# Optimization experiments

Measured on AMD Instinct MI355X. Metric: run time of the kernel, lower is better.

## Reference

```python
import jax, jax.numpy as jnp
import numpy as np

NOT_EPSILON = 1.0
W_SCALE = 0.05  # scaled randn init for numerical stability of swishmax logits

H, T, A, C = 8, 1024, 64, 256  # heads, key/query size, attention size, compress size


def swishmax(x, axis):
    m = jnp.max(x, axis=axis, keepdims=True)
    xe = x * jnp.exp(x - m)
    return xe / (jnp.sum(jnp.abs(xe), axis=axis, keepdims=True) + NOT_EPSILON)


def setup_inputs() -> dict:
    key = jax.random.key(0)
    ks = jax.random.split(key, 7)
    B, Q, K = 2, 2048, 2048
    return {
        "query_tokens": jax.random.normal(ks[0], (B, Q, T), dtype=jnp.float32),
        "key_tokens": jax.random.normal(ks[1], (B, K, T), dtype=jnp.float32),
        "key_down": jax.random.normal(ks[2], (H, T, A), dtype=jnp.float32) * W_SCALE,
        "query_down": jax.random.normal(ks[3], (H, T, A), dtype=jnp.float32) * W_SCALE,
        "query_down_bias": jax.random.normal(ks[4], (H, 1, A), dtype=jnp.float32) * W_SCALE,
        "value_down": jax.random.normal(ks[5], (H, T, C), dtype=jnp.float32) * W_SCALE,
        "value_up": jax.random.normal(ks[6], (H, C, T), dtype=jnp.float32) * W_SCALE,
    }


def reference(query_tokens, key_tokens, key_down, query_down, query_down_bias, value_down, value_up):
    # key/query projections: [B,K,T] x [H,T,A] -> [B,H,K,A]
    k = jnp.einsum('bkt,hta->bhka', key_tokens, key_down)
    q = jnp.einsum('bqt,hta->bhqa', query_tokens, query_down) + query_down_bias[None]  # [B,H,Q,A]
    # attention logits: key @ query^T -> [B,H,K,Q]
    logits = jnp.einsum('bhka,bhqa->bhkq', k, q)
    attn = swishmax(logits, axis=-2)  # normalized over keys (dim=-2)
    # sum_k key_tokens[b,k,:] * attn[b,h,k,q]  ==  [B,H,Q,T] (matmul form of the outer-product sum)
    vs = jnp.einsum('bhkq,bkt->bhqt', attn, key_tokens)
    # compress path: value_down then value_up
    vs = jnp.einsum('bhqc,hct->bhqt', jnp.einsum('bhqt,htc->bhqc', vs, value_down), value_up)
    return vs.sum(axis=1)  # sum over heads -> [B,Q,T]
```

## Files before the change

### kernel.cpp

```cpp
#include <hip/hip_runtime.h>
#include <hip/hip_fp16.h>
#include <math.h>


typedef _Float16 f16;
typedef _Float16 f16x4 __attribute__((ext_vector_type(4)));
typedef _Float16 f16x8 __attribute__((ext_vector_type(8)));
typedef short s16x4 __attribute__((ext_vector_type(4)));
typedef short bf16x8 __attribute__((ext_vector_type(8)));
typedef float f32x4 __attribute__((ext_vector_type(4)));

#define MFMA_F16(a, b, c) __builtin_amdgcn_mfma_f32_16x16x32_f16(a, b, c, 0, 0, 0)
#define MFMA_BF16(a, b, c) __builtin_amdgcn_mfma_f32_16x16x32_bf16(a, b, c, 0, 0, 0)

__device__ __forceinline__ void g2lds16(const void* g, void* l) {
  __builtin_amdgcn_global_load_lds((__attribute__((address_space(1))) void*)g,
                                   (__attribute__((address_space(3))) void*)l, 16, 0, 0);
}

__device__ __forceinline__ short f32_bf16(float x) {
  union { float f; unsigned u; } v; v.f = x;
  unsigned r = v.u + 0x7FFFu + ((v.u >> 16) & 1u);
  return (short)(r >> 16);
}
__device__ __forceinline__ float bf16_f32(short h) {
  union { unsigned u; float f; } v; v.u = ((unsigned)(unsigned short)h) << 16;
  return v.f;
}

__global__ __launch_bounds__(256) void ew_split(const float* __restrict__ in,
                                                short* __restrict__ bhi,
                                                short* __restrict__ blo,
                                                f16* __restrict__ fo, int n4) {
  int i = blockIdx.x * 256 + threadIdx.x;
  int stride = gridDim.x * 256;
  for (; i < n4; i += stride) {
    f32x4 v = ((const f32x4*)in)[i];
    s16x4 h, l;
    f16x4 f;
#pragma unroll
    for (int j = 0; j < 4; j++) {
      short hj = f32_bf16(v[j]);
      h[j] = hj;
      l[j] = f32_bf16(v[j] - bf16_f32(hj));
      f[j] = (f16)v[j];
    }
    ((s16x4*)bhi)[i] = h;
    ((s16x4*)blo)[i] = l;
    if (fo) ((f16x4*)fo)[i] = f;
  }
}

__global__ __launch_bounds__(256) void transpose_split(const float* __restrict__ in,
                                                       short* __restrict__ bhi,
                                                       short* __restrict__ blo,
                                                       f16* __restrict__ fo,
                                                       int R, int C) {
  __shared__ float t[64][65];
  int cb = blockIdx.x * 64, rb = blockIdx.y * 64;
  size_t batch = (size_t)blockIdx.z * R * C;
  int tid = threadIdx.x;
#pragma unroll
  for (int i = 0; i < 4; i++) {
    int r = (tid >> 4) + i * 16, c4 = (tid & 15) * 4;
    f32x4 v = *(const f32x4*)(in + batch + (size_t)(rb + r) * C + cb + c4);
    t[r][c4] = v[0]; t[r][c4 + 1] = v[1]; t[r][c4 + 2] = v[2]; t[r][c4 + 3] = v[3];
  }
  __syncthreads();
#pragma unroll
  for (int i = 0; i < 4; i++) {
    int c = (tid >> 4) + i * 16, r4 = (tid & 15) * 4;
    float v0 = t[r4][c], v1 = t[r4 + 1][c], v2 = t[r4 + 2][c], v3 = t[r4 + 3][c];
    size_t o = batch + (size_t)(cb + c) * R + rb + r4;
    if (bhi) {
      s16x4 h = {f32_bf16(v0), f32_bf16(v1), f32_bf16(v2), f32_bf16(v3)};
      *(s16x4*)(bhi + o) = h;
      s16x4 l = {f32_bf16(v0 - bf16_f32(h[0])), f32_bf16(v1 - bf16_f32(h[1])),
                 f32_bf16(v2 - bf16_f32(h[2])), f32_bf16(v3 - bf16_f32(h[3]))};
      *(s16x4*)(blo + o) = l;
    }
    if (fo) {
      f16x4 fv = {(f16)v0, (f16)v1, (f16)v2, (f16)v3};
      *(f16x4*)(fo + o) = fv;
    }
  }
}

__global__ __launch_bounds__(256, 2) void proj_gemm(
    const short* __restrict__ qtok_hi, const short* __restrict__ qtok_lo,
    const short* __restrict__ ktok_hi, const short* __restrict__ ktok_lo,
    const short* __restrict__ wqT_hi, const short* __restrict__ wqT_lo,
    const short* __restrict__ wkT_hi, const short* __restrict__ wkT_lo,
    const float* __restrict__ bias, short* __restrict__ q_split,
    short* __restrict__ k_split) {
  const bool isQ = (blockIdx.z == 0);
  const short* Ahi = isQ ? qtok_hi : ktok_hi;
  const short* Alo = isQ ? qtok_lo : ktok_lo;
  const short* Bhi = isQ ? wqT_hi : wkT_hi;
  const short* Blo = isQ ? wqT_lo : wkT_lo;
  short* outp = isQ ? q_split : k_split;

  __shared__ __attribute__((aligned(16))) short sm[2][12288];

  int tid = threadIdx.x, w = tid >> 6, lane = tid & 63, g = lane >> 4, li = lane & 15;
  int mb = blockIdx.y * 64, nb = blockIdx.x * 128;
  int wm = (w >> 1) * 32, wn = (w & 1) * 64;

  f32x4 acc[2][4] = {};

  auto STAGE = [&](int kb, int buf) {
    {
      int off = tid * 16;
      int row = off >> 6, ss = ((off >> 4) & 3) ^ ((row >> 1) & 3);
      size_t src = (size_t)(mb + row) * 1024 + kb + ss * 8;
      g2lds16(Ahi + src, (char*)&sm[buf][0] + w * 1024);
      g2lds16(Alo + src, (char*)&sm[buf][2048] + w * 1024);
    }
#pragma unroll
    for (int i = 0; i < 2; i++) {
      int off = i * 4096 + tid * 16;
      int row = off >> 6, ss = ((off >> 4) & 3) ^ ((row >> 1) & 3);
      size_t src = (size_t)(nb + row) * 1024 + kb + ss * 8;
      g2lds16(Bhi + src, (char*)&sm[buf][4096] + i * 4096 + w * 1024);
      g2lds16(Blo + src, (char*)&sm[buf][8192] + i * 4096 + w * 1024);
    }
  };

  STAGE(0, 0);
  __syncthreads();
  for (int kb = 0; kb < 1024; kb += 32) {
    int cur = (kb >> 5) & 1;
    if (kb + 32 < 1024) STAGE(kb + 32, cur ^ 1);
    bf16x8 af[2][2], bf[4][2];
#pragma unroll
    for (int f = 0; f < 2; f++) {
      int ra = wm + f * 16 + li, sa = g ^ ((ra >> 1) & 3);
      af[f][0] = *(const bf16x8*)&sm[cur][ra * 32 + sa * 8];
      af[f][1] = *(const bf16x8*)&sm[cur][2048 + ra * 32 + sa * 8];
    }
#pragma unroll
    for (int f = 0; f < 4; f++) {
      int rb = wn + f * 16 + li, sb = g ^ ((rb >> 1) & 3);
      bf[f][0] = *(const bf16x8*)&sm[cur][4096 + rb * 32 + sb * 8];
      bf[f][1] = *(const bf16x8*)&sm[cur][8192 + rb * 32 + sb * 8];
    }
#pragma unroll
    for (int mf = 0; mf < 2; mf++)
#pragma unroll
      for (int nf = 0; nf < 4; nf++) {
        acc[mf][nf] = MFMA_BF16(af[mf][0], bf[nf][0], acc[mf][nf]);
        acc[mf][nf] = MFMA_BF16(af[mf][0], bf[nf][1], acc[mf][nf]);
        acc[mf][nf] = MFMA_BF16(af[mf][1], bf[nf][0], acc[mf][nf]);
      }
    __syncthreads();
  }
#pragma unroll
  for (int mf = 0; mf < 2; mf++)
#pragma unroll
    for (int nf = 0; nf < 4; nf++)
#pragma unroll
      for (int r = 0; r < 4; r++) {
        int m = mb + wm + mf * 16 + 4 * g + r;
        int n = nb + wn + nf * 16 + li;
        float v = acc[mf][nf][r];
        if (isQ) v += bias[n];
        short hi = f32_bf16(v);
        short lo = f32_bf16(v - bf16_f32(hi));
        size_t base = ((size_t)((m >> 11) * 8 + (n >> 6)) * 2048 + (m & 2047)) * 128;
        outp[base + (n & 63)] = hi;
        outp[base + 64 + (n & 63)] = lo;
      }
}

__global__ __launch_bounds__(256, 4) void kv_gemm(const f16* __restrict__ A,
                                                  const f16* __restrict__ Bm,
                                                  f16* __restrict__ kvT) {
  __shared__ __attribute__((aligned(16))) f16 sm[2][6144];
  int tid = threadIdx.x, w = tid >> 6, lane = tid & 63, g = lane >> 4, li = lane & 15;
  int mb = blockIdx.y * 64, nb = blockIdx.x * 128;
  int wm = (w >> 1) * 32, wn = (w & 1) * 64;
  f32x4 acc[2][4] = {};

  auto STAGE = [&](int kb, int buf) {
    {
      int off = tid * 16;
      int row = off >> 6, ss = ((off >> 4) & 3) ^ ((row >> 1) & 3);
      g2lds16(A + (size_t)(mb + row) * 1024 + kb + ss * 8, (char*)&sm[buf][0] + w * 1024);
    }
#pragma unroll
    for (int i = 0; i < 2; i++) {
      int off = i * 4096 + tid * 16;
      int row = off >> 6, ss = ((off >> 4) & 3) ^ ((row >> 1) & 3);
      g2lds16(Bm + (size_t)(nb + row) * 1024 + kb + ss * 8,
              (char*)&sm[buf][2048] + i * 4096 + w * 1024);
    }
  };

  STAGE(0, 0);
  __syncthreads();
  for (int kb = 0; kb < 1024; kb += 32) {
    int cur = (kb >> 5) & 1;
    if (kb + 32 < 1024) STAGE(kb + 32, cur ^ 1);
    f16x8 af[2], bf[4];
#pragma unroll
    for (int f = 0; f < 2; f++) {
      int ra = wm + f * 16 + li, sa = g ^ ((ra >> 1) & 3);
      af[f] = *(const f16x8*)&sm[cur][ra * 32 + sa * 8];
    }
#pragma unroll
    for (int f = 0; f < 4; f++) {
      int rb = wn + f * 16 + li, sb = g ^ ((rb >> 1) & 3);
      bf[f] = *(const f16x8*)&sm[cur][2048 + rb * 32 + sb * 8];
    }
#pragma unroll
    for (int mf = 0; mf < 2; mf++)
#pragma unroll
      for (int nf = 0; nf < 4; nf++)
        acc[mf][nf] = MFMA_F16(af[mf], bf[nf], acc[mf][nf]);
    __syncthreads();
  }
#pragma unroll
  for (int mf = 0; mf < 2; mf++)
#pragma unroll
    for (int nf = 0; nf < 4; nf++) {
      int m = mb + wm + mf * 16 + 4 * g;
      int n = nb + wn + nf * 16 + li;
      f16x4 v = {(f16)acc[mf][nf][0], (f16)acc[mf][nf][1], (f16)acc[mf][nf][2],
                 (f16)acc[mf][nf][3]};
      int bh = (m >> 11) * 8 + (n >> 8);
      size_t o = (size_t)bh * 524288 + (size_t)((m & 2047) >> 5) * 8192 +
                 (size_t)(n & 255) * 32 + (m & 31);
      *(f16x4*)(kvT + o) = v;
    }
}

__global__ __launch_bounds__(256, 2) void flash_attn(const short* __restrict__ q_split,
                                                     const short* __restrict__ k_split,
                                                     const f16* __restrict__ kvT,
                                                     f16* __restrict__ vs_c) {
  __shared__ __attribute__((aligned(16))) short k_lds[2][4096];
  __shared__ __attribute__((aligned(16))) f16 kv_lds[2][8192];
  __shared__ __attribute__((aligned(16))) f16 p_lds[2][4096];
  __shared__ float sc_lds[2][4][16];
  __shared__ float fix_lds[64];

  const int bid = blockIdx.x;
  const int bh = ((bid & 7) << 1) + ((bid >> 3) & 1);
  const int qb = bid >> 4;
  const int tid = threadIdx.x;
  const int w = tid >> 6, lane = tid & 63, g = lane >> 4, li = lane & 15;

  const short* qrow = q_split + ((size_t)bh * 2048 + qb * 64 + w * 16 + li) * 128;
  bf16x8 qf[2][2];
#pragma unroll
  for (int ach = 0; ach < 2; ach++)
#pragma unroll
    for (int hl = 0; hl < 2; hl++)
      qf[ach][hl] = *(const bf16x8*)(qrow + hl * 64 + ach * 32 + g * 8);

  const short* kbase = k_split + (size_t)bh * 262144;
  const f16* kvbase = kvT + (size_t)bh * 524288;

  float m_cur = -INFINITY, m_true = -INFINITY, l_run = 0.f;
  f32x4 acc[4][4] = {};

  auto STAGE_K = [&](int kt, int buf) {
#pragma unroll
    for (int i = 0; i < 2; i++) {
      int off = (w * 2 + i) * 1024 + lane * 16;
      int row = off >> 8;
      int ss = ((off >> 4) & 15) ^ (row & 7);
      g2lds16(kbase + kt * 4096 + row * 128 + ss * 8,
              (char*)k_lds[buf] + (w * 2 + i) * 1024);
    }
  };
  auto STAGE_KV = [&](int kt, int buf) {
#pragma unroll
    for (int i = 0; i < 4; i++) {
      int off = (w * 4 + i) * 1024 + lane * 16;
      int c = off >> 6;
      int ss = ((off >> 4) & 3) ^ ((c >> 1) & 3);
      g2lds16(kvbase + kt * 8192 + c * 32 + ss * 8,
              (char*)kv_lds[buf] + (w * 4 + i) * 1024);
    }
  };

  auto QKSM = [&](int buf) {
    f32x4 s[2] = {};
    __builtin_amdgcn_s_setprio(1);
#pragma unroll
    for (int kc = 0; kc < 2; kc++) {
      const int r = kc * 16 + li;
#pragma unroll
      for (int ach = 0; ach < 2; ach++) {
        int sh = (ach * 4 + g) ^ (r & 7);
        int sl = (8 + ach * 4 + g) ^ (r & 7);
        bf16x8 khi = *(const bf16x8*)((const char*)k_lds[buf] + r * 256 + sh * 16);
        bf16x8 klo = *(const bf16x8*)((const char*)k_lds[buf] + r * 256 + sl * 16);
        s[kc] = MFMA_BF16(khi, qf[ach][0], s[kc]);
        s[kc] = MFMA_BF16(khi, qf[ach][1], s[kc]);
        s[kc] = MFMA_BF16(klo, qf[ach][0], s[kc]);
      }
    }
    __builtin_amdgcn_s_setprio(0);

    float tmax = fmaxf(fmaxf(fmaxf(s[0][0], s[0][1]), fmaxf(s[0][2], s[0][3])),
                       fmaxf(fmaxf(s[1][0], s[1][1]), fmaxf(s[1][2], s[1][3])));
    tmax = fmaxf(tmax, __shfl_xor(tmax, 16));
    tmax = fmaxf(tmax, __shfl_xor(tmax, 32));
    m_true = fmaxf(m_true, tmax);
    float sc = 1.0f;
    if (__any(tmax > m_cur + 4.0f)) {
      float mn = fmaxf(m_cur, tmax);
      sc = __expf(m_cur - mn);
      l_run *= sc;
      m_cur = mn;
    }
    if (g == 0) sc_lds[buf][w][li] = sc;

    float ls = 0.f;
    float pv[8];
#pragma unroll
    for (int kc = 0; kc < 2; kc++)
#pragma unroll
      for (int r2 = 0; r2 < 4; r2++) {
        float sv = s[kc][r2];
        float e = sv * __expf(sv - m_cur);
        pv[kc * 4 + r2] = e;
        ls += fabsf(e);
      }
    ls += __shfl_xor(ls, 16);
    ls += __shfl_xor(ls, 32);
    l_run += ls;

#pragma unroll
    for (int kc = 0; kc < 2; kc++) {
      f16x4 p4 = {(f16)pv[kc * 4], (f16)pv[kc * 4 + 1], (f16)pv[kc * 4 + 2],
                  (f16)pv[kc * 4 + 3]};
      int wb = ((w * 16 + li) * 128 + kc * 32 + g * 8) ^ ((li & 7) << 4);
      *(f16x4*)((char*)p_lds[buf] + wb) = p4;
    }
  };

  STAGE_K(0, 0);
  STAGE_KV(0, 0);
  STAGE_K(1, 1);
  __syncthreads();
  QKSM(0);

#pragma unroll 2
  for (int kt = 0; kt < 64; kt++) {
    const int cur = kt & 1;
    __syncthreads();
    if (kt < 63) STAGE_KV(kt + 1, cur ^ 1);
    if (kt < 62) STAGE_K(kt + 2, cur);

    f16x8 kvf[4];
#pragma unroll
    for (int ct = 0; ct < 4; ct++) {
      int c = w * 64 + ct * 16 + li;
      int ss = g ^ ((c >> 1) & 3);
      kvf[ct] = *(const f16x8*)((const char*)kv_lds[cur] + c * 64 + ss * 16);
    }

    if (kt < 63) QKSM(cur ^ 1);

#pragma unroll
    for (int qt = 0; qt < 4; qt++) {
      float scq = sc_lds[cur][qt][li];
      if (__any(scq != 1.0f)) {
#pragma unroll
        for (int ct = 0; ct < 4; ct++) acc[ct][qt] *= scq;
      }
    }

    __builtin_amdgcn_s_setprio(1);
#pragma unroll
    for (int qt = 0; qt < 4; qt++) {
      int rb = ((qt * 16 + li) * 128 + g * 16) ^ ((li & 7) << 4);
      f16x8 pf = *(const f16x8*)((const char*)p_lds[cur] + rb);
#pragma unroll
      for (int ct = 0; ct < 4; ct++) acc[ct][qt] = MFMA_F16(kvf[ct], pf, acc[ct][qt]);
    }
    __builtin_amdgcn_s_setprio(0);
  }

  float sfix = __expf(m_cur - m_true);
  float invd = sfix / (l_run * sfix + 1.0f);
  __syncthreads();
  if (g == 0) fix_lds[w * 16 + li] = invd;
  __syncthreads();
#pragma unroll
  for (int qt = 0; qt < 4; qt++) {
    float iv = fix_lds[qt * 16 + li];
    f16* orow = vs_c + ((size_t)(bh >> 3) * 2048 + qb * 64 + qt * 16 + li) * 2048 +
                (bh & 7) * 256 + w * 64 + g * 4;
#pragma unroll
    for (int ct = 0; ct < 4; ct++) {
      f16x4 v = {(f16)(acc[ct][qt][0] * iv), (f16)(acc[ct][qt][1] * iv),
                 (f16)(acc[ct][qt][2] * iv), (f16)(acc[ct][qt][3] * iv)};
      *(f16x4*)(orow + ct * 16) = v;
    }
  }
}

__global__ __launch_bounds__(256, 2) void final_gemm(const f16* __restrict__ A,
                                                     const f16* __restrict__ Bm,
                                                     float* __restrict__ outp) {
  __shared__ __attribute__((aligned(16))) f16 sm[2][6144];
  int tid = threadIdx.x, w = tid >> 6, lane = tid & 63, g = lane >> 4, li = lane & 15;
  int mb = blockIdx.y * 64, nb = blockIdx.x * 128;
  int wm = (w >> 1) * 32, wn = (w & 1) * 64;
  f32x4 acc[2][4] = {};

  auto STAGE = [&](int kb, int buf) {
    {
      int off = tid * 16;
      int row = off >> 6, ss = ((off >> 4) & 3) ^ ((row >> 1) & 3);
      g2lds16(A + (size_t)(mb + row) * 2048 + kb + ss * 8, (char*)&sm[buf][0] + w * 1024);
    }
#pragma unroll
    for (int i = 0; i < 2; i++) {
      int off = i * 4096 + tid * 16;
      int row = off >> 6, ss = ((off >> 4) & 3) ^ ((row >> 1) & 3);
      g2lds16(Bm + (size_t)(nb + row) * 2048 + kb + ss * 8,
              (char*)&sm[buf][2048] + i * 4096 + w * 1024);
    }
  };

  STAGE(0, 0);
  __syncthreads();
  for (int kb = 0; kb < 2048; kb += 32) {
    int cur = (kb >> 5) & 1;
    if (kb + 32 < 2048) STAGE(kb + 32, cur ^ 1);
    f16x8 af[2], bf[4];
#pragma unroll
    for (int f = 0; f < 2; f++) {
      int ra = wm + f * 16 + li, sa = g ^ ((ra >> 1) & 3);
      af[f] = *(const f16x8*)&sm[cur][ra * 32 + sa * 8];
    }
#pragma unroll
    for (int f = 0; f < 4; f++) {
      int rb = wn + f * 16 + li, sb = g ^ ((rb >> 1) & 3);
      bf[f] = *(const f16x8*)&sm[cur][2048 + rb * 32 + sb * 8];
    }
#pragma unroll
    for (int mf = 0; mf < 2; mf++)
#pragma unroll
      for (int nf = 0; nf < 4; nf++)
        acc[mf][nf] = MFMA_F16(af[mf], bf[nf], acc[mf][nf]);
    __syncthreads();
  }
#pragma unroll
  for (int mf = 0; mf < 2; mf++)
#pragma unroll
    for (int nf = 0; nf < 4; nf++)
#pragma unroll
      for (int r = 0; r < 4; r++) {
        int m = mb + wm + mf * 16 + 4 * g + r;
        int n = nb + wn + nf * 16 + li;
        outp[(size_t)m * 1024 + n] = acc[mf][nf][r];
      }
}

extern "C" void kernel_launch(void* const* d_in, const int* in_sizes, int n_in,
                              void* d_out, int out_size, void* d_ws, size_t ws_size,
                              hipStream_t stream) {
  (void)in_sizes; (void)n_in; (void)out_size; (void)ws_size;
  const float* qtok = (const float*)d_in[0];
  const float* ktok = (const float*)d_in[1];
  const float* kdw = (const float*)d_in[2];
  const float* qdw = (const float*)d_in[3];
  const float* qdb = (const float*)d_in[4];
  const float* vdw = (const float*)d_in[5];
  const float* vup = (const float*)d_in[6];

  char* ws = (char*)d_ws;
  size_t off = 0;
  auto take = [&](size_t n) { void* p = ws + off; off += (n + 255) & ~(size_t)255; return p; };

  short* qtok_hi = (short*)take(8u << 20);
  short* qtok_lo = (short*)take(8u << 20);
  short* ktok_hi = (short*)take(8u << 20);
  short* ktok_lo = (short*)take(8u << 20);
  f16* ktok_f = (f16*)take(8u << 20);
  short* wqT_hi = (short*)take(1u << 20);
  short* wqT_lo = (short*)take(1u << 20);
  short* wkT_hi = (short*)take(1u << 20);
  short* wkT_lo = (short*)take(1u << 20);
  f16* vdT = (f16*)take(4u << 20);
  f16* vuT = (f16*)take(4u << 20);
  short* q_split = (short*)take(8u << 20);
  short* k_split = (short*)take(8u << 20);
  f16* kvT = (f16*)(void*)ktok_hi;
  f16* vs_c = (f16*)(void*)qtok_hi;

  ew_split<<<2048, 256, 0, stream>>>(qtok, qtok_hi, qtok_lo, (f16*)nullptr, 1048576);
  ew_split<<<2048, 256, 0, stream>>>(ktok, ktok_hi, ktok_lo, ktok_f, 1048576);
  transpose_split<<<dim3(1, 16, 8), 256, 0, stream>>>(qdw, wqT_hi, wqT_lo, nullptr, 1024, 64);
  transpose_split<<<dim3(1, 16, 8), 256, 0, stream>>>(kdw, wkT_hi, wkT_lo, nullptr, 1024, 64);
  transpose_split<<<dim3(4, 16, 8), 256, 0, stream>>>(vdw, nullptr, nullptr, vdT, 1024, 256);
  transpose_split<<<dim3(16, 32, 1), 256, 0, stream>>>(vup, nullptr, nullptr, vuT, 2048, 1024);

  proj_gemm<<<dim3(4, 64, 2), 256, 0, stream>>>(qtok_hi, qtok_lo, ktok_hi, ktok_lo,
                                                wqT_hi, wqT_lo, wkT_hi, wkT_lo, qdb,
                                                q_split, k_split);
  kv_gemm<<<dim3(16, 64), 256, 0, stream>>>(ktok_f, vdT, kvT);
  flash_attn<<<512, 256, 0, stream>>>(q_split, k_split, kvT, vs_c);
  final_gemm<<<dim3(8, 64), 256, 0, stream>>>(vs_c, vuT, (float*)d_out);
}
```

Measured before the change: 228.0 us.

## Load KV fragments directly to registers, double key tile, fuse preprocessing launches

```diff
diff --git a/kernel.cpp b/kernel.cpp
--- a/kernel.cpp
+++ b/kernel.cpp
@@ -28,37 +28,69 @@
   return v.f;
 }
 
-__global__ __launch_bounds__(256) void ew_split(const float* __restrict__ in,
-                                                short* __restrict__ bhi,
-                                                short* __restrict__ blo,
-                                                f16* __restrict__ fo, int n4) {
+__global__ __launch_bounds__(256) void ew_split2(const float* __restrict__ qin,
+                                                 const float* __restrict__ kin,
+                                                 short* __restrict__ qhi,
+                                                 short* __restrict__ qlo,
+                                                 short* __restrict__ khi,
+                                                 short* __restrict__ klo,
+                                                 f16* __restrict__ kf) {
   int i = blockIdx.x * 256 + threadIdx.x;
-  int stride = gridDim.x * 256;
-  for (; i < n4; i += stride) {
-    f32x4 v = ((const f32x4*)in)[i];
-    s16x4 h, l;
-    f16x4 f;
-#pragma unroll
-    for (int j = 0; j < 4; j++) {
-      short hj = f32_bf16(v[j]);
-      h[j] = hj;
-      l[j] = f32_bf16(v[j] - bf16_f32(hj));
-      f[j] = (f16)v[j];
-    }
-    ((s16x4*)bhi)[i] = h;
-    ((s16x4*)blo)[i] = l;
-    if (fo) ((f16x4*)fo)[i] = f;
-  }
-}
-
-__global__ __launch_bounds__(256) void transpose_split(const float* __restrict__ in,
-                                                       short* __restrict__ bhi,
-                                                       short* __restrict__ blo,
-                                                       f16* __restrict__ fo,
-                                                       int R, int C) {
+  const bool isK = i >= 1048576;
+  const int j = isK ? i - 1048576 : i;
+  const float* in = isK ? kin : qin;
+  f32x4 v = ((const f32x4*)in)[j];
+  s16x4 h, l;
+  f16x4 f;
+#pragma unroll
+  for (int e = 0; e < 4; e++) {
+    short he = f32_bf16(v[e]);
+    h[e] = he;
+    l[e] = f32_bf16(v[e] - bf16_f32(he));
+    f[e] = (f16)v[e];
+  }
+  if (isK) {
+    ((s16x4*)khi)[j] = h;
+    ((s16x4*)klo)[j] = l;
+    ((f16x4*)kf)[j] = f;
+  } else {
+    ((s16x4*)qhi)[j] = h;
+    ((s16x4*)qlo)[j] = l;
+  }
+}
+
+__global__ __launch_bounds__(256) void transpose_all(
+    const float* __restrict__ qdw, const float* __restrict__ kdw,
+    const float* __restrict__ vdw, const float* __restrict__ vup,
+    short* __restrict__ wqT_hi, short* __restrict__ wqT_lo,
+    short* __restrict__ wkT_hi, short* __restrict__ wkT_lo,
+    f16* __restrict__ vdT, f16* __restrict__ vuT) {
   __shared__ float t[64][65];
-  int cb = blockIdx.x * 64, rb = blockIdx.y * 64;
-  size_t batch = (size_t)blockIdx.z * R * C;
+  int idx = blockIdx.x;
+  const float* in;
+  short *bhi = nullptr, *blo = nullptr;
+  f16* fo = nullptr;
+  int R, C, cb, rb;
+  size_t batch;
+  if (idx < 256) {
+    bool isQ = idx < 128;
+    int i = isQ ? idx : idx - 128;
+    in = isQ ? qdw : kdw;
+    bhi = isQ ? wqT_hi : wkT_hi;
+    blo = isQ ? wqT_lo : wkT_lo;
+    R = 1024; C = 64; cb = 0; rb = (i & 15) * 64;
+    batch = (size_t)(i >> 4) * R * C;
+  } else if (idx < 768) {
+    int i = idx - 256;
+    in = vdw; fo = vdT;
+    R = 1024; C = 256; cb = (i & 3) * 64; rb = ((i >> 2) & 15) * 64;
+    batch = (size_t)(i >> 6) * R * C;
+  } else {
+    int i = idx - 768;
+    in = vup; fo = vuT;
+    R = 2048; C = 1024; cb = (i & 15) * 64; rb = (i >> 4) * 64;
+    batch = 0;
+  }
   int tid = threadIdx.x;
 #pragma unroll
   for (int i = 0; i < 4; i++) {
@@ -238,8 +270,7 @@
                                                      const short* __restrict__ k_split,
                                                      const f16* __restrict__ kvT,
                                                      f16* __restrict__ vs_c) {
-  __shared__ __attribute__((aligned(16))) short k_lds[2][4096];
-  __shared__ __attribute__((aligned(16))) f16 kv_lds[2][8192];
+  __shared__ __attribute__((aligned(16))) short k_lds[2][8192];
   __shared__ __attribute__((aligned(16))) f16 p_lds[2][4096];
   __shared__ float sc_lds[2][4][16];
   __shared__ float fix_lds[64];
@@ -259,37 +290,37 @@
       qf[ach][hl] = *(const bf16x8*)(qrow + hl * 64 + ach * 32 + g * 8);
 
   const short* kbase = k_split + (size_t)bh * 262144;
-  const f16* kvbase = kvT + (size_t)bh * 524288;
+  const f16* kvbase = kvT + (size_t)bh * 524288 + (size_t)w * 64 * 32 + li * 32 + g * 8;
 
   float m_cur = -INFINITY, m_true = -INFINITY, l_run = 0.f;
   f32x4 acc[4][4] = {};
-
-  auto STAGE_K = [&](int kt, int buf) {
-#pragma unroll
-    for (int i = 0; i < 2; i++) {
-      int off = (w * 2 + i) * 1024 + lane * 16;
+  f16x8 kvf[2][4];
+
+  auto STAGE_K = [&](int t, int buf) {
+#pragma unroll
+    for (int i = 0; i < 4; i++) {
+      int off = (w * 4 + i) * 1024 + lane * 16;
       int row = off >> 8;
       int ss = ((off >> 4) & 15) ^ (row & 7);
-      g2lds16(kbase + kt * 4096 + row * 128 + ss * 8,
-              (char*)k_lds[buf] + (w * 2 + i) * 1024);
+      g2lds16(kbase + t * 8192 + row * 128 + ss * 8,
+              (char*)k_lds[buf] + (w * 4 + i) * 1024);
     }
   };
-  auto STAGE_KV = [&](int kt, int buf) {
-#pragma unroll
-    for (int i = 0; i < 4; i++) {
-      int off = (w * 4 + i) * 1024 + lane * 16;
-      int c = off >> 6;
-      int ss = ((off >> 4) & 3) ^ ((c >> 1) & 3);
-      g2lds16(kvbase + kt * 8192 + c * 32 + ss * 8,
-              (char*)kv_lds[buf] + (w * 4 + i) * 1024);
+
+  auto LOADKV = [&](int t) {
+#pragma unroll
+    for (int h = 0; h < 2; h++) {
+      const f16* p = kvbase + (size_t)(2 * t + h) * 8192;
+#pragma unroll
+      for (int ct = 0; ct < 4; ct++) kvf[h][ct] = *(const f16x8*)(p + ct * 512);
     }
   };
 
   auto QKSM = [&](int buf) {
-    f32x4 s[2] = {};
+    f32x4 s[4] = {};
     __builtin_amdgcn_s_setprio(1);
 #pragma unroll
-    for (int kc = 0; kc < 2; kc++) {
+    for (int kc = 0; kc < 4; kc++) {
       const int r = kc * 16 + li;
 #pragma unroll
       for (int ach = 0; ach < 2; ach++) {
@@ -304,8 +335,10 @@
     }
     __builtin_amdgcn_s_setprio(0);
 
-    float tmax = fmaxf(fmaxf(fmaxf(s[0][0], s[0][1]), fmaxf(s[0][2], s[0][3])),
-                       fmaxf(fmaxf(s[1][0], s[1][1]), fmaxf(s[1][2], s[1][3])));
+    float tmax = -INFINITY;
+#pragma unroll
+    for (int kc = 0; kc < 4; kc++)
+      tmax = fmaxf(tmax, fmaxf(fmaxf(s[kc][0], s[kc][1]), fmaxf(s[kc][2], s[kc][3])));
     tmax = fmaxf(tmax, __shfl_xor(tmax, 16));
     tmax = fmaxf(tmax, __shfl_xor(tmax, 32));
     m_true = fmaxf(m_true, tmax);
@@ -319,9 +352,9 @@
     if (g == 0) sc_lds[buf][w][li] = sc;
 
     float ls = 0.f;
-    float pv[8];
-#pragma unroll
-    for (int kc = 0; kc < 2; kc++)
+    float pv[16];
+#pragma unroll
+    for (int kc = 0; kc < 4; kc++)
 #pragma unroll
       for (int r2 = 0; r2 < 4; r2++) {
         float sv = s[kc][r2];
@@ -334,7 +367,7 @@
     l_run += ls;
 
 #pragma unroll
-    for (int kc = 0; kc < 2; kc++) {
+    for (int kc = 0; kc < 4; kc++) {
       f16x4 p4 = {(f16)pv[kc * 4], (f16)pv[kc * 4 + 1], (f16)pv[kc * 4 + 2],
                   (f16)pv[kc * 4 + 3]};
       int wb = ((w * 16 + li) * 128 + kc * 32 + g * 8) ^ ((li & 7) << 4);
@@ -343,27 +376,17 @@
   };
 
   STAGE_K(0, 0);
-  STAGE_KV(0, 0);
   STAGE_K(1, 1);
   __syncthreads();
   QKSM(0);
 
 #pragma unroll 2
-  for (int kt = 0; kt < 64; kt++) {
-    const int cur = kt & 1;
+  for (int t = 0; t < 32; t++) {
+    const int cur = t & 1;
     __syncthreads();
-    if (kt < 63) STAGE_KV(kt + 1, cur ^ 1);
-    if (kt < 62) STAGE_K(kt + 2, cur);
-
-    f16x8 kvf[4];
-#pragma unroll
-    for (int ct = 0; ct < 4; ct++) {
-      int c = w * 64 + ct * 16 + li;
-      int ss = g ^ ((c >> 1) & 3);
-      kvf[ct] = *(const f16x8*)((const char*)kv_lds[cur] + c * 64 + ss * 16);
-    }
-
-    if (kt < 63) QKSM(cur ^ 1);
+    LOADKV(t);
+    if (t < 30) STAGE_K(t + 2, cur);
+    if (t < 31) QKSM(cur ^ 1);
 
 #pragma unroll
     for (int qt = 0; qt < 4; qt++) {
@@ -377,10 +400,14 @@
     __builtin_amdgcn_s_setprio(1);
 #pragma unroll
     for (int qt = 0; qt < 4; qt++) {
-      int rb = ((qt * 16 + li) * 128 + g * 16) ^ ((li & 7) << 4);
-      f16x8 pf = *(const f16x8*)((const char*)p_lds[cur] + rb);
-#pragma unroll
-      for (int ct = 0; ct < 4; ct++) acc[ct][qt] = MFMA_F16(kvf[ct], pf, acc[ct][qt]);
+#pragma unroll
+      for (int h = 0; h < 2; h++) {
+        int rb = ((qt * 16 + li) * 128 + h * 64 + g * 16) ^ ((li & 7) << 4);
+        f16x8 pf = *(const f16x8*)((const char*)p_lds[cur] + rb);
+#pragma unroll
+        for (int ct = 0; ct < 4; ct++)
+          acc[ct][qt] = MFMA_F16(kvf[h][ct], pf, acc[ct][qt]);
+      }
     }
     __builtin_amdgcn_s_setprio(0);
   }
@@ -495,13 +522,10 @@
   f16* kvT = (f16*)(void*)ktok_hi;
   f16* vs_c = (f16*)(void*)qtok_hi;
 
-  ew_split<<<2048, 256, 0, stream>>>(qtok, qtok_hi, qtok_lo, (f16*)nullptr, 1048576);
-  ew_split<<<2048, 256, 0, stream>>>(ktok, ktok_hi, ktok_lo, ktok_f, 1048576);
-  transpose_split<<<dim3(1, 16, 8), 256, 0, stream>>>(qdw, wqT_hi, wqT_lo, nullptr, 1024, 64);
-  transpose_split<<<dim3(1, 16, 8), 256, 0, stream>>>(kdw, wkT_hi, wkT_lo, nullptr, 1024, 64);
-  transpose_split<<<dim3(4, 16, 8), 256, 0, stream>>>(vdw, nullptr, nullptr, vdT, 1024, 256);
-  transpose_split<<<dim3(16, 32, 1), 256, 0, stream>>>(vup, nullptr, nullptr, vuT, 2048, 1024);
-
+  ew_split2<<<8192, 256, 0, stream>>>(qtok, ktok, qtok_hi, qtok_lo, ktok_hi,
+                                      ktok_lo, ktok_f);
+  transpose_all<<<1280, 256, 0, stream>>>(qdw, kdw, vdw, vup, wqT_hi, wqT_lo,
+                                          wkT_hi, wkT_lo, vdT, vuT);
   proj_gemm<<<dim3(4, 64, 2), 256, 0, stream>>>(qtok_hi, qtok_lo, ktok_hi, ktok_lo,
                                                 wqT_hi, wqT_lo, wkT_hi, wkT_lo, qdb,
                                                 q_split, k_split);
```

Result: faster. 203.3 us (-10.8%).
